# Kernel optimization log

Hardware: AMD Instinct MI355X
Metric: run time of the kernel (lower is better)

The kernel has to match this reference:

```python
import jax, jax.numpy as jnp
import numpy as np

B, S, F = 16, 4096, 1024


def setup_inputs() -> dict:
    key = jax.random.key(0)
    k_units, k_mask = jax.random.split(key)
    units = jax.random.normal(k_units, (B, S, F), dtype=jnp.float32)
    mask = jax.random.randint(k_mask, (B, S), 0, 2, dtype=jnp.int32)
    return {"units": units, "mask": mask}


def reference(units, mask):
    # units: [B, S, F] subtoken features; mask: [B, S] 0/1 token-beginning flags.
    # Output: [B, T, F] where T = max token count per row; features of masked
    # subtokens are packed left-aligned per row, remainder zero-padded.
    b, s, f = units.shape
    token_lens = jnp.sum(mask, axis=1)                # [B]
    T = int(jnp.max(token_lens))                      # data-dependent pad length (eager)
    m = mask.astype(bool)
    # destination token slot of each subtoken within its row (0-based)
    pos = jnp.cumsum(mask.astype(jnp.int32), axis=1) - 1   # [B, S]
    # route non-token subtokens to a dump slot T (sliced off below)
    pos = jnp.where(m, pos, T)
    batch_idx = jnp.arange(b, dtype=jnp.int32)[:, None]    # [B, 1]
    out = jnp.zeros((b, T + 1, f), dtype=units.dtype)
    out = out.at[batch_idx, pos].set(units)
    return out[:, :T, :]
```

## Files before the change

kernel.cpp:

```cpp
#include <hip/hip_runtime.h>

#define B_ 16
#define S_ 4096
#define F_ 1024
#define F4_ (F_ / 4)
#define ROWS_ 8

__global__ __launch_bounds__(1024) void pos_kernel(const int* __restrict__ mask,
                                                   int* __restrict__ src,
                                                   int* __restrict__ lens) {
    const int b   = blockIdx.x;
    const int tid = threadIdx.x;

    const int4 m = ((const int4*)(mask + b * S_))[tid];
    const int local = m.x + m.y + m.z + m.w;

    const int lane = tid & 63;
    const int wid  = tid >> 6;

    int incl = local;
#pragma unroll
    for (int d = 1; d < 64; d <<= 1) {
        int n = __shfl_up(incl, d, 64);
        if (lane >= d) incl += n;
    }

    __shared__ int wsum[16];
    __shared__ int woff[16];
    if (lane == 63) wsum[wid] = incl;
    __syncthreads();
    if (wid == 0) {
        int v = (lane < 16) ? wsum[lane] : 0;
        int iscan = v;
#pragma unroll
        for (int d = 1; d < 16; d <<= 1) {
            int n = __shfl_up(iscan, d, 64);
            if (lane >= d) iscan += n;
        }
        if (lane < 16) woff[lane] = iscan - v;
        if (lane == 15) lens[b] = iscan;
    }
    __syncthreads();

    int p = woff[wid] + (incl - local);
    const int s0 = tid * 4;
    int* srow = src + b * S_;
    if (m.x) srow[p++] = s0;
    if (m.y) srow[p++] = s0 + 1;
    if (m.z) srow[p++] = s0 + 2;
    if (m.w) srow[p]   = s0 + 3;
}

__global__ __launch_bounds__(F4_) void scatter_kernel(const float4* __restrict__ units,
                                                      const int* __restrict__ src,
                                                      const int* __restrict__ lens,
                                                      float4* __restrict__ out, int T) {
    const int b  = blockIdx.y;
    const int t0 = blockIdx.x * ROWS_;
    const int len = lens[b];
    const int* srow = src + b * S_;

    float4 v[ROWS_];
    const float4 zero = make_float4(0.f, 0.f, 0.f, 0.f);
#pragma unroll
    for (int i = 0; i < ROWS_; ++i) {
        const int t = t0 + i;
        if (t < len) {
            const int s = srow[t];
            v[i] = units[((size_t)(b * S_ + s)) * F4_ + threadIdx.x];
        } else {
            v[i] = zero;
        }
    }

    const size_t obase = ((size_t)b * (size_t)T + t0) * F4_ + threadIdx.x;
#pragma unroll
    for (int i = 0; i < ROWS_; ++i) {
        if (t0 + i < T) out[obase + (size_t)i * F4_] = v[i];
    }
}

extern "C" void kernel_launch(void* const* d_in, const int* in_sizes, int n_in,
                              void* d_out, int out_size, void* d_ws, size_t ws_size,
                              hipStream_t stream) {
    const float* units = (const float*)d_in[0];
    const int*   mask  = (const int*)d_in[1];
    float*       out   = (float*)d_out;

    const int T = out_size / (B_ * F_);

    int* src  = (int*)d_ws;
    int* lens = src + B_ * S_;

    pos_kernel<<<B_, 1024, 0, stream>>>(mask, src, lens);

    dim3 grid((unsigned)((T + ROWS_ - 1) / ROWS_), B_);
    scatter_kernel<<<grid, F4_, 0, stream>>>((const float4*)units, src, lens,
                                             (float4*)out, T);
}
```

Before: 55.65 us.

## Fuse mask prefix scan into scatter kernel, recomputing positions per block

Removes the separate position kernel and its global src/lens workspace. Each scatter block re-reads its row's 4096-entry mask, runs a block-wide prefix scan, and records only the source indices for its 8 output rows in shared memory before gathering. This drops one launch and the dependency between the two kernels. In exchange, every block now does a redundant 16 KB mask read and scan, which adds latency before any gather starts.

Result: faster. 53.70 us (-3.5%).

```diff
diff --git a/kernel.cpp b/kernel.cpp
--- a/kernel.cpp
+++ b/kernel.cpp
@@ -5,18 +5,26 @@
 #define F_ 1024
 #define F4_ (F_ / 4)
 #define ROWS_ 8
+#define NT_ 256
+#define EPT_ (S_ / NT_)
 
-__global__ __launch_bounds__(1024) void pos_kernel(const int* __restrict__ mask,
-                                                   int* __restrict__ src,
-                                                   int* __restrict__ lens) {
-    const int b   = blockIdx.x;
+__global__ __launch_bounds__(NT_) void fused_kernel(const float4* __restrict__ units,
+                                                    const int* __restrict__ mask,
+                                                    float4* __restrict__ out, int T) {
+    const int b   = blockIdx.y;
+    const int t0  = blockIdx.x * ROWS_;
     const int tid = threadIdx.x;
-
-    const int4 m = ((const int4*)(mask + b * S_))[tid];
-    const int local = m.x + m.y + m.z + m.w;
-
     const int lane = tid & 63;
     const int wid  = tid >> 6;
+
+    const int4* mrow = (const int4*)(mask + b * S_);
+    int4 m[EPT_ / 4];
+#pragma unroll
+    for (int k = 0; k < EPT_ / 4; ++k) m[k] = mrow[tid * (EPT_ / 4) + k];
+
+    int local = 0;
+#pragma unroll
+    for (int k = 0; k < EPT_ / 4; ++k) local += m[k].x + m[k].y + m[k].z + m[k].w;
 
     int incl = local;
 #pragma unroll
@@ -25,40 +33,37 @@
         if (lane >= d) incl += n;
     }
 
-    __shared__ int wsum[16];
-    __shared__ int woff[16];
+    __shared__ int wsum[4];
+    __shared__ int woff[4];
+    __shared__ int slen;
+    __shared__ int ssrc[ROWS_];
     if (lane == 63) wsum[wid] = incl;
     __syncthreads();
-    if (wid == 0) {
-        int v = (lane < 16) ? wsum[lane] : 0;
-        int iscan = v;
+    if (tid == 0) {
+        int acc = 0;
 #pragma unroll
-        for (int d = 1; d < 16; d <<= 1) {
-            int n = __shfl_up(iscan, d, 64);
-            if (lane >= d) iscan += n;
-        }
-        if (lane < 16) woff[lane] = iscan - v;
-        if (lane == 15) lens[b] = iscan;
+        for (int w = 0; w < 4; ++w) { woff[w] = acc; acc += wsum[w]; }
+        slen = acc;
     }
     __syncthreads();
 
-    int p = woff[wid] + (incl - local);
-    const int s0 = tid * 4;
-    int* srow = src + b * S_;
-    if (m.x) srow[p++] = s0;
-    if (m.y) srow[p++] = s0 + 1;
-    if (m.z) srow[p++] = s0 + 2;
-    if (m.w) srow[p]   = s0 + 3;
-}
+    int r = woff[wid] + (incl - local);
+    const int s0 = tid * EPT_;
+#pragma unroll
+    for (int k = 0; k < EPT_ / 4; ++k) {
+        const int mv[4] = {m[k].x, m[k].y, m[k].z, m[k].w};
+#pragma unroll
+        for (int j = 0; j < 4; ++j) {
+            if (mv[j]) {
+                const unsigned rel = (unsigned)(r - t0);
+                if (rel < (unsigned)ROWS_) ssrc[rel] = s0 + k * 4 + j;
+                ++r;
+            }
+        }
+    }
+    __syncthreads();
 
-__global__ __launch_bounds__(F4_) void scatter_kernel(const float4* __restrict__ units,
-                                                      const int* __restrict__ src,
-                                                      const int* __restrict__ lens,
-                                                      float4* __restrict__ out, int T) {
-    const int b  = blockIdx.y;
-    const int t0 = blockIdx.x * ROWS_;
-    const int len = lens[b];
-    const int* srow = src + b * S_;
+    const int len = slen;
 
     float4 v[ROWS_];
     const float4 zero = make_float4(0.f, 0.f, 0.f, 0.f);
@@ -66,14 +71,14 @@
     for (int i = 0; i < ROWS_; ++i) {
         const int t = t0 + i;
         if (t < len) {
-            const int s = srow[t];
-            v[i] = units[((size_t)(b * S_ + s)) * F4_ + threadIdx.x];
+            const int s = ssrc[i];
+            v[i] = units[((size_t)(b * S_ + s)) * F4_ + tid];
         } else {
             v[i] = zero;
         }
     }
 
-    const size_t obase = ((size_t)b * (size_t)T + t0) * F4_ + threadIdx.x;
+    const size_t obase = ((size_t)b * (size_t)T + t0) * F4_ + tid;
 #pragma unroll
     for (int i = 0; i < ROWS_; ++i) {
         if (t0 + i < T) out[obase + (size_t)i * F4_] = v[i];
@@ -89,12 +94,7 @@
 
     const int T = out_size / (B_ * F_);
 
-    int* src  = (int*)d_ws;
-    int* lens = src + B_ * S_;
-
-    pos_kernel<<<B_, 1024, 0, stream>>>(mask, src, lens);
-
     dim3 grid((unsigned)((T + ROWS_ - 1) / ROWS_), B_);
-    scatter_kernel<<<grid, F4_, 0, stream>>>((const float4*)units, src, lens,
-                                             (float4*)out, T);
+    fused_kernel<<<grid, NT_, 0, stream>>>((const float4*)units, mask,
+                                           (float4*)out, T);
 }
```
